# Optimization experiments

Hardware: AMD Instinct MI355X
Metric: run time of the kernel (lower is better)

Reference implementation:

```python
import jax, jax.numpy as jnp
import numpy as np

D_MODEL = 1024
NHEAD = 16
D_HEAD = D_MODEL // NHEAD


def setup_inputs() -> dict:
    key = jax.random.key(0)
    ks = jax.random.split(key, 5)
    s_in = 1.0 / np.sqrt(D_MODEL)
    x = jax.random.normal(ks[0], (2, 2048, D_MODEL), dtype=jnp.float32)
    Wqkv = jax.random.uniform(ks[1], (D_MODEL, 3 * D_MODEL), jnp.float32, -s_in, s_in)
    bqkv = jax.random.uniform(ks[2], (3 * D_MODEL,), jnp.float32, -s_in, s_in)
    Wproj = jax.random.uniform(ks[3], (D_MODEL, D_MODEL), jnp.float32, -s_in, s_in)
    bproj = jax.random.uniform(ks[4], (D_MODEL,), jnp.float32, -s_in, s_in)
    return {"x": x, "Wqkv": Wqkv, "bqkv": bqkv, "Wproj": Wproj, "bproj": bproj}


def reference(x, Wqkv, bqkv, Wproj, bproj):
    B, N, D = x.shape
    qkv = x @ Wqkv + bqkv                       # [B, N, 3D]
    q, k, v = jnp.split(qkv, 3, axis=-1)
    # [B, N, D] -> [B, H, N, d]
    def to_heads(t):
        return t.reshape(B, N, NHEAD, D_HEAD).transpose(0, 2, 1, 3)
    q, k, v = to_heads(q), to_heads(k), to_heads(v)
    scale = 1.0 / np.sqrt(D_HEAD).astype(np.float32)
    attn = jnp.einsum('bhqd,bhkd->bhqk', q, k) * scale
    attn = jax.nn.softmax(attn, axis=-1)
    y = jnp.einsum('bhqk,bhkd->bhqd', attn, v)  # [B, H, N, d]
    y = y.transpose(0, 2, 1, 3).reshape(B, N, D)
    return y @ Wproj + bproj
```

## Files before the change

### kernel.cpp

```cpp
#include <hip/hip_runtime.h>
#include <hip/hip_bf16.h>
#include <stdint.h>

typedef __hip_bfloat16 bf16;
typedef __attribute__((ext_vector_type(8))) short short8;
typedef __attribute__((ext_vector_type(4))) float f32x4;

#define QSCALE 0.18033688011f

__device__ __forceinline__ float fast_exp2(float x) {
#if __has_builtin(__builtin_amdgcn_exp2f)
  return __builtin_amdgcn_exp2f(x);
#else
  return exp2f(x);
#endif
}

__device__ __forceinline__ uint32_t pack2_bf16(float a, float b) {
#if __has_builtin(__builtin_amdgcn_cvt_pk_bf16_f32)
  typedef __attribute__((ext_vector_type(2))) __bf16 bf16x2;
  bf16x2 v = __builtin_amdgcn_cvt_pk_bf16_f32(a, b);
  return __builtin_bit_cast(uint32_t, v);
#else
  uint32_t ua = __builtin_bit_cast(uint32_t, a);
  uint32_t ub = __builtin_bit_cast(uint32_t, b);
  ua += 0x7FFF + ((ua >> 16) & 1);
  ub += 0x7FFF + ((ub >> 16) & 1);
  return (ua >> 16) | (ub & 0xFFFF0000u);
#endif
}

__device__ __forceinline__ void gload_lds16(const bf16* g, bf16* l) {
#if __has_builtin(__builtin_amdgcn_global_load_lds)
  __builtin_amdgcn_global_load_lds(
      (const __attribute__((address_space(1))) void*)(uintptr_t)g,
      (__attribute__((address_space(3))) void*)(uint32_t)(uintptr_t)l,
      16, 0, 0);
#else
  int lane = threadIdx.x & 63;
  *(short8*)(l + lane * 8) = *(const short8*)(g + lane * 8);
#endif
}

__device__ __forceinline__ void lds_barrier() {
  asm volatile("s_waitcnt lgkmcnt(0)\n\ts_barrier" ::: "memory");
}

__device__ __forceinline__ void transpose_tile(const float* __restrict__ in,
                                               bf16* __restrict__ out,
                                               int R, int C, int bx, int by,
                                               bf16 (*t)[72]) {
  const int r0 = by * 64, c0 = bx * 64;
  const int rr = threadIdx.x >> 3, cc = (threadIdx.x & 7) * 8;
#pragma unroll
  for (int rep = 0; rep < 2; ++rep) {
    int y = rr + rep * 32;
    const float* p = in + (size_t)(r0 + y) * C + c0 + cc;
    f32x4 v0 = *(const f32x4*)p;
    f32x4 v1 = *(const f32x4*)(p + 4);
#pragma unroll
    for (int j = 0; j < 4; ++j) {
      t[cc + j][y] = __float2bfloat16(v0[j]);
      t[cc + 4 + j][y] = __float2bfloat16(v1[j]);
    }
  }
  __syncthreads();
#pragma unroll
  for (int rep = 0; rep < 2; ++rep) {
    int y = rr + rep * 32;
    short8 v = *(const short8*)&t[y][cc];
    *(short8*)(out + (size_t)(c0 + y) * R + r0 + cc) = v;
  }
}

__global__ __launch_bounds__(256)
void prep_k(const float* __restrict__ x, bf16* __restrict__ xb,
            const float* __restrict__ Wqkv, bf16* __restrict__ WtQkv,
            const float* __restrict__ Wproj, bf16* __restrict__ WtP) {
  __shared__ __align__(16) bf16 t[64][72];
  const int bid = blockIdx.x;
  if (bid < 2048) {
    int i = (bid * 256 + threadIdx.x) * 8;
    f32x4 v0 = *(const f32x4*)(x + i);
    f32x4 v1 = *(const f32x4*)(x + i + 4);
    short8 r;
    bf16* rb = (bf16*)&r;
#pragma unroll
    for (int j = 0; j < 4; ++j) {
      rb[j] = __float2bfloat16(v0[j]);
      rb[4 + j] = __float2bfloat16(v1[j]);
    }
    *(short8*)(xb + i) = r;
  } else if (bid < 2048 + 768) {
    int b = bid - 2048;
    transpose_tile(Wqkv, WtQkv, 1024, 3072, b % 48, b / 48, t);
  } else {
    int b = bid - 2816;
    transpose_tile(Wproj, WtP, 1024, 1024, b % 16, b / 16, t);
  }
}

template <int MODE, int TM>
__global__ __launch_bounds__(256, 2)
void gemm_bt(const bf16* __restrict__ A, const bf16* __restrict__ Bt,
             const float* __restrict__ bias, float* __restrict__ outp,
             bf16* __restrict__ Qd, bf16* __restrict__ Kd, bf16* __restrict__ Vt,
             int M, int Nn, int K) {
  constexpr int MI = TM / 32;
  __shared__ __align__(16) bf16 As[TM * 32];
  __shared__ __align__(16) bf16 Bs[128 * 32];

  const int tid = threadIdx.x;
  const int wave = tid >> 6, lane = tid & 63;
  const int quad = lane >> 4, l16 = lane & 15;
  const int mw = (wave >> 1) * (TM / 2), nw = (wave & 1) * 64;
  const int m_blk = blockIdx.y * TM, n_blk = blockIdx.x * 128;

  f32x4 acc[MI][4];
#pragma unroll
  for (int i = 0; i < MI; ++i)
#pragma unroll
    for (int j = 0; j < 4; ++j) acc[i][j] = (f32x4){0.f, 0.f, 0.f, 0.f};

  const int rowA = lane >> 2, colA = (lane & 3) * 8;
  const int chunkB = wave * 2;
  const bf16* gB = Bt + (size_t)(n_blk + chunkB * 16 + rowA) * K + colA;
  bf16* lB0 = &Bs[chunkB * 16 * 32];
  bf16* lB1 = &Bs[(chunkB + 1) * 16 * 32];

  const int chunkA = (TM == 128) ? wave * 2 : wave;
  const bf16* gA = A + (size_t)(m_blk + chunkA * 16 + rowA) * K + colA;
  bf16* lA0 = &As[chunkA * 16 * 32];
  bf16* lA1 = &As[(chunkA + 1) * 16 * 32];

  for (int kt = 0; kt < K; kt += 32) {
    gload_lds16(gA, lA0);
    if (TM == 128) gload_lds16(gA + 16 * K, lA1);
    gload_lds16(gB, lB0);
    gload_lds16(gB + 16 * K, lB1);
    gA += 32; gB += 32;
    __syncthreads();
    short8 af[MI], bfv[4];
#pragma unroll
    for (int i = 0; i < MI; ++i)
      af[i] = *(const short8*)&As[(mw + i * 16 + l16) * 32 + quad * 8];
#pragma unroll
    for (int j = 0; j < 4; ++j)
      bfv[j] = *(const short8*)&Bs[(nw + j * 16 + l16) * 32 + quad * 8];
#pragma unroll
    for (int i = 0; i < MI; ++i)
#pragma unroll
      for (int j = 0; j < 4; ++j)
        acc[i][j] = __builtin_amdgcn_mfma_f32_16x16x32_bf16(af[i], bfv[j],
                                                            acc[i][j], 0, 0, 0);
    __syncthreads();
  }

#pragma unroll
  for (int j = 0; j < 4; ++j) {
    const int ncol = n_blk + nw + j * 16 + l16;
    const float bval = bias[ncol];
    if (MODE == 0) {
      const int part = ncol >> 10;
      const int rem = ncol & 1023;
      const int h = rem >> 6, dh = rem & 63;
#pragma unroll
      for (int i = 0; i < MI; ++i) {
        const int t0 = m_blk + mw + i * 16 + quad * 4;
        const int b = t0 >> 11, tt = t0 & 2047;
        const size_t bh = (size_t)(b * 16 + h);
        if (part == 2) {
          uint32_t w0 = pack2_bf16(acc[i][j][0] + bval, acc[i][j][1] + bval);
          uint32_t w1 = pack2_bf16(acc[i][j][2] + bval, acc[i][j][3] + bval);
          uint2 pk; pk.x = w0; pk.y = w1;
          *(uint2*)&Vt[(bh * 64 + dh) * 2048 + tt] = pk;
        } else {
          bf16* dst = (part == 0) ? Qd : Kd;
          const float sc = (part == 0) ? QSCALE : 1.0f;
#pragma unroll
          for (int r = 0; r < 4; ++r)
            dst[(bh * 2048 + tt + r) * 64 + dh] =
                __float2bfloat16((acc[i][j][r] + bval) * sc);
        }
      }
    } else {
#pragma unroll
      for (int i = 0; i < MI; ++i) {
        const int mrow0 = m_blk + mw + i * 16 + quad * 4;
#pragma unroll
        for (int r = 0; r < 4; ++r)
          outp[(size_t)(mrow0 + r) * Nn + ncol] = acc[i][j][r] + bval;
      }
    }
  }
}

__global__ __launch_bounds__(256, 3)
void attn_kernel(const bf16* __restrict__ Qg, const bf16* __restrict__ Kg,
                 const bf16* __restrict__ Vt, bf16* __restrict__ yg) {
  __shared__ __align__(16) bf16 Ks[2][64][72];
  __shared__ __align__(16) bf16 Vts[2][64 * 72];
  __shared__ __align__(16) bf16 Ps[64][72];

  const int tid = threadIdx.x;
  const int wave = tid >> 6, lane = tid & 63;
  const int quad = lane >> 4, l16 = lane & 15;
  const int qh = wave & 1, kvh = wave >> 1;

  const int bx = blockIdx.x;
  const int qt = bx & 31;
  const int bh = bx >> 5;

  const bf16* Qb = Qg + ((size_t)bh * 2048 + qt * 64) * 64;
  const bf16* Kb = Kg + (size_t)bh * 2048 * 64;
  const bf16* Vtb = Vt + (size_t)bh * 64 * 2048;

  short8 qf[2][2];
#pragma unroll
  for (int qblk = 0; qblk < 2; ++qblk)
#pragma unroll
    for (int kb = 0; kb < 2; ++kb)
      qf[qblk][kb] = *(const short8*)(
          Qb + (size_t)(qh * 32 + qblk * 16 + l16) * 64 + kb * 32 + quad * 8);

  f32x4 yacc[2][4];
#pragma unroll
  for (int qblk = 0; qblk < 2; ++qblk)
#pragma unroll
    for (int dblk = 0; dblk < 4; ++dblk)
      yacc[qblk][dblk] = (f32x4){0.f, 0.f, 0.f, 0.f};
  float sum_l[2] = {0.f, 0.f};

  const int kr = tid >> 3, kc = (tid & 7) * 8;
  const int vdd = tid & 63, vo = tid >> 6;
  const int voff0 = vdd * 72 + (((vo) + (vdd >> 3)) & 7) * 8;
  const int voff1 = vdd * 72 + (((vo + 4) + (vdd >> 3)) & 7) * 8;
  const bf16* Kp0 = Kb + (size_t)kr * 64 + kc;
  const bf16* Kp1 = Kb + (size_t)(kr + 32) * 64 + kc;
  const bf16* Vp0 = Vtb + (size_t)vdd * 2048 + vo * 8;
  const bf16* Vp1 = Vtb + (size_t)vdd * 2048 + (vo + 4) * 8;

  {
    short8 a = *(const short8*)Kp0;
    short8 b = *(const short8*)Kp1;
    short8 c = *(const short8*)Vp0;
    short8 d = *(const short8*)Vp1;
    *(short8*)&Ks[0][kr][kc] = a;
    *(short8*)&Ks[0][kr + 32][kc] = b;
    *(short8*)&Vts[0][voff0] = c;
    *(short8*)&Vts[0][voff1] = d;
  }
  short8 gk0 = *(const short8*)(Kp0 + (size_t)64 * 64);
  short8 gk1 = *(const short8*)(Kp1 + (size_t)64 * 64);
  short8 gv0 = *(const short8*)(Vp0 + 64);
  short8 gv1 = *(const short8*)(Vp1 + 64);
  __syncthreads();

  for (int kt = 0; kt < 2048; kt += 64) {
    const int cur = (kt >> 6) & 1;

    if (kt + 64 < 2048) {
      *(short8*)&Ks[cur ^ 1][kr][kc] = gk0;
      *(short8*)&Ks[cur ^ 1][kr + 32][kc] = gk1;
      *(short8*)&Vts[cur ^ 1][voff0] = gv0;
      *(short8*)&Vts[cur ^ 1][voff1] = gv1;
      if (kt + 128 < 2048) {
        gk0 = *(const short8*)(Kp0 + (size_t)(kt + 128) * 64);
        gk1 = *(const short8*)(Kp1 + (size_t)(kt + 128) * 64);
        gv0 = *(const short8*)(Vp0 + kt + 128);
        gv1 = *(const short8*)(Vp1 + kt + 128);
      }
    }

    f32x4 st[2][2];
#pragma unroll
    for (int kvblk = 0; kvblk < 2; ++kvblk) {
      const int krow = kvh * 32 + kvblk * 16 + l16;
      short8 kf0 = *(const short8*)&Ks[cur][krow][quad * 8];
      short8 kf1 = *(const short8*)&Ks[cur][krow][32 + quad * 8];
#pragma unroll
      for (int qblk = 0; qblk < 2; ++qblk) {
        f32x4 a = (f32x4){0.f, 0.f, 0.f, 0.f};
        a = __builtin_amdgcn_mfma_f32_16x16x32_bf16(kf0, qf[qblk][0], a, 0, 0, 0);
        a = __builtin_amdgcn_mfma_f32_16x16x32_bf16(kf1, qf[qblk][1], a, 0, 0, 0);
        st[qblk][kvblk] = a;
      }
    }

#pragma unroll
    for (int qblk = 0; qblk < 2; ++qblk) {
      float ssum = 0.f;
#pragma unroll
      for (int kvblk = 0; kvblk < 2; ++kvblk) {
        float p0 = fast_exp2(st[qblk][kvblk][0]);
        float p1 = fast_exp2(st[qblk][kvblk][1]);
        float p2 = fast_exp2(st[qblk][kvblk][2]);
        float p3 = fast_exp2(st[qblk][kvblk][3]);
        ssum += (p0 + p1) + (p2 + p3);
        uint2 pk;
        pk.x = pack2_bf16(p0, p1);
        pk.y = pack2_bf16(p2, p3);
        *(uint2*)&Ps[qh * 32 + qblk * 16 + l16]
                    [kvh * 32 + kvblk * 16 + quad * 4] = pk;
      }
      sum_l[qblk] += ssum;
    }

    lds_barrier();

    short8 vbf[4];
#pragma unroll
    for (int dblk = 0; dblk < 4; ++dblk) {
      const int d = dblk * 16 + l16;
      vbf[dblk] = *(const short8*)&Vts[cur][d * 72 +
          (((kvh * 4 + quad) + (d >> 3)) & 7) * 8];
    }
#pragma unroll
    for (int qblk = 0; qblk < 2; ++qblk) {
      short8 pa = *(const short8*)&Ps[qh * 32 + qblk * 16 + l16]
                                     [kvh * 32 + quad * 8];
#pragma unroll
      for (int dblk = 0; dblk < 4; ++dblk)
        yacc[qblk][dblk] = __builtin_amdgcn_mfma_f32_16x16x32_bf16(
            pa, vbf[dblk], yacc[qblk][dblk], 0, 0, 0);
    }

    lds_barrier();
  }

#pragma unroll
  for (int qblk = 0; qblk < 2; ++qblk) {
    sum_l[qblk] += __shfl_xor(sum_l[qblk], 16);
    sum_l[qblk] += __shfl_xor(sum_l[qblk], 32);
  }
  __syncthreads();
  float* red = (float*)&Ks[0][0][0];
  float* sred = (float*)&Ps[0][0];
  if (kvh == 1) {
#pragma unroll
    for (int qblk = 0; qblk < 2; ++qblk) {
#pragma unroll
      for (int dblk = 0; dblk < 4; ++dblk) {
        const int f = (qh * 2 + qblk) * 4 + dblk;
        *(f32x4*)&red[(f * 64 + quad * 16 + l16) * 4] = yacc[qblk][dblk];
      }
      if (quad == 0) sred[(qh * 2 + qblk) * 16 + l16] = sum_l[qblk];
    }
  }
  __syncthreads();
  if (kvh == 0) {
    const int b = bh >> 4, h = bh & 15;
    const size_t rowbase = (size_t)b * 2048 + qt * 64;
#pragma unroll
    for (int qblk = 0; qblk < 2; ++qblk) {
      sum_l[qblk] += sred[(qh * 2 + qblk) * 16 + l16];
#pragma unroll
      for (int dblk = 0; dblk < 4; ++dblk) {
        const int f = (qh * 2 + qblk) * 4 + dblk;
        f32x4 o = *(const f32x4*)&red[(f * 64 + quad * 16 + l16) * 4];
#pragma unroll
        for (int r = 0; r < 4; ++r) yacc[qblk][dblk][r] += o[r];
      }
#pragma unroll
      for (int r = 0; r < 4; ++r) {
        const float lv = __shfl(sum_l[qblk], quad * 4 + r, 16);
        const float inv = 1.f / lv;
        const int rr = qh * 32 + qblk * 16 + quad * 4 + r;
#pragma unroll
        for (int dblk = 0; dblk < 4; ++dblk)
          yg[(rowbase + rr) * 1024 + h * 64 + dblk * 16 + l16] =
              __float2bfloat16(yacc[qblk][dblk][r] * inv);
      }
    }
  }
}

extern "C" void kernel_launch(void* const* d_in, const int* in_sizes, int n_in,
                              void* d_out, int out_size, void* d_ws, size_t ws_size,
                              hipStream_t stream) {
  const float* x = (const float*)d_in[0];
  const float* Wqkv = (const float*)d_in[1];
  const float* bqkv = (const float*)d_in[2];
  const float* Wproj = (const float*)d_in[3];
  const float* bproj = (const float*)d_in[4];
  float* out = (float*)d_out;

  if (ws_size < (size_t)40 * 1024 * 1024) return;

  char* ws = (char*)d_ws;
  bf16* xb    = (bf16*)(ws + 0);
  bf16* yd    = (bf16*)(ws + 0);
  bf16* WtQkv = (bf16*)(ws + 8388608);
  bf16* WtP   = (bf16*)(ws + 14680064);
  bf16* Qd    = (bf16*)(ws + 16777216);
  bf16* Kd    = (bf16*)(ws + 25165824);
  bf16* Vten  = (bf16*)(ws + 33554432);

  prep_k<<<3072, 256, 0, stream>>>(x, xb, Wqkv, WtQkv, Wproj, WtP);
  gemm_bt<0, 128><<<dim3(24, 32), 256, 0, stream>>>(
      xb, WtQkv, bqkv, nullptr, Qd, Kd, Vten, 4096, 3072, 1024);
  attn_kernel<<<dim3(1024), 256, 0, stream>>>(Qd, Kd, Vten, yd);
  gemm_bt<1, 64><<<dim3(8, 64), 256, 0, stream>>>(
      yd, WtP, bproj, out, nullptr, nullptr, nullptr, 4096, 1024, 1024);
}
```

Before: 200.6 us.

## Stage QKV GEMM epilogue through LDS for coalesced stores; single-buffer K in attention

The QKV GEMM epilogue now writes each head's tile into shared memory, then stores Q/K rows and transposed V rows to global memory with 16-byte coalesced writes, replacing scattered 2-byte and 8-byte stores. The attention kernel drops K double-buffering: K is written into a single LDS buffer after the QK barrier. This frees LDS so the occupancy hint can rise from 3 to 4 blocks. The cost is extra barriers and LDS traffic in the epilogue, and a shorter window to hide K load latency.

```diff
diff --git a/kernel.cpp b/kernel.cpp
--- a/kernel.cpp
+++ b/kernel.cpp
@@ -107,8 +107,9 @@
              bf16* __restrict__ Qd, bf16* __restrict__ Kd, bf16* __restrict__ Vt,
              int M, int Nn, int K) {
   constexpr int MI = TM / 32;
-  __shared__ __align__(16) bf16 As[TM * 32];
-  __shared__ __align__(16) bf16 Bs[128 * 32];
+  __shared__ __align__(16) bf16 smem[(TM == 128) ? 9216 : 6144];
+  bf16* As = smem;
+  bf16* Bs = smem + TM * 32;
 
   const int tid = threadIdx.x;
   const int wave = tid >> 6, lane = tid & 63;
@@ -156,34 +157,73 @@
     __syncthreads();
   }
 
-#pragma unroll
-  for (int j = 0; j < 4; ++j) {
-    const int ncol = n_blk + nw + j * 16 + l16;
-    const float bval = bias[ncol];
-    if (MODE == 0) {
-      const int part = ncol >> 10;
-      const int rem = ncol & 1023;
-      const int h = rem >> 6, dh = rem & 63;
-#pragma unroll
-      for (int i = 0; i < MI; ++i) {
-        const int t0 = m_blk + mw + i * 16 + quad * 4;
-        const int b = t0 >> 11, tt = t0 & 2047;
-        const size_t bh = (size_t)(b * 16 + h);
+  if (MODE == 0) {
+    float bval[4];
+#pragma unroll
+    for (int j = 0; j < 4; ++j) bval[j] = bias[n_blk + nw + j * 16 + l16];
+
+    const int part = n_blk >> 10;
+    const int b = m_blk >> 11;
+    const int tloc = m_blk & 2047;
+    const int h0 = (n_blk & 1023) >> 6;
+
+#pragma unroll
+    for (int p = 0; p < 2; ++p) {
+      __syncthreads();
+      if ((nw >> 6) == p) {
         if (part == 2) {
-          uint32_t w0 = pack2_bf16(acc[i][j][0] + bval, acc[i][j][1] + bval);
-          uint32_t w1 = pack2_bf16(acc[i][j][2] + bval, acc[i][j][3] + bval);
-          uint2 pk; pk.x = w0; pk.y = w1;
-          *(uint2*)&Vt[(bh * 64 + dh) * 2048 + tt] = pk;
+#pragma unroll
+          for (int i = 0; i < MI; ++i)
+#pragma unroll
+            for (int j = 0; j < 4; ++j) {
+              const int dh = j * 16 + l16;
+              const int t0 = mw + i * 16 + quad * 4;
+              uint2 pk;
+              pk.x = pack2_bf16(acc[i][j][0] + bval[j], acc[i][j][1] + bval[j]);
+              pk.y = pack2_bf16(acc[i][j][2] + bval[j], acc[i][j][3] + bval[j]);
+              *(uint2*)&smem[dh * 136 + t0] = pk;
+            }
         } else {
-          bf16* dst = (part == 0) ? Qd : Kd;
           const float sc = (part == 0) ? QSCALE : 1.0f;
 #pragma unroll
-          for (int r = 0; r < 4; ++r)
-            dst[(bh * 2048 + tt + r) * 64 + dh] =
-                __float2bfloat16((acc[i][j][r] + bval) * sc);
+          for (int i = 0; i < MI; ++i)
+#pragma unroll
+            for (int j = 0; j < 4; ++j) {
+              const int d = j * 16 + l16;
+              const int t0 = mw + i * 16 + quad * 4;
+#pragma unroll
+              for (int r = 0; r < 4; ++r)
+                smem[(t0 + r) * 72 + d] =
+                    __float2bfloat16((acc[i][j][r] + bval[j]) * sc);
+            }
         }
       }
-    } else {
+      __syncthreads();
+      const size_t bh = (size_t)(b * 16 + h0 + p);
+      if (part == 2) {
+#pragma unroll
+        for (int it = 0; it < 4; ++it) {
+          const int dl = (tid >> 4) + it * 16;
+          const int t8 = (tid & 15) * 8;
+          short8 v = *(const short8*)&smem[dl * 136 + t8];
+          *(short8*)&Vt[(bh * 64 + dl) * 2048 + tloc + t8] = v;
+        }
+      } else {
+        bf16* dst = (part == 0) ? Qd : Kd;
+#pragma unroll
+        for (int it = 0; it < 4; ++it) {
+          const int row = (tid >> 3) + it * 32;
+          const int col8 = (tid & 7) * 8;
+          short8 v = *(const short8*)&smem[row * 72 + col8];
+          *(short8*)&dst[(bh * 2048 + tloc + row) * 64 + col8] = v;
+        }
+      }
+    }
+  } else {
+#pragma unroll
+    for (int j = 0; j < 4; ++j) {
+      const int ncol = n_blk + nw + j * 16 + l16;
+      const float bval = bias[ncol];
 #pragma unroll
       for (int i = 0; i < MI; ++i) {
         const int mrow0 = m_blk + mw + i * 16 + quad * 4;
@@ -195,10 +235,10 @@
   }
 }
 
-__global__ __launch_bounds__(256, 3)
+__global__ __launch_bounds__(256, 4)
 void attn_kernel(const bf16* __restrict__ Qg, const bf16* __restrict__ Kg,
                  const bf16* __restrict__ Vt, bf16* __restrict__ yg) {
-  __shared__ __align__(16) bf16 Ks[2][64][72];
+  __shared__ __align__(16) bf16 Ks[64][72];
   __shared__ __align__(16) bf16 Vts[2][64 * 72];
   __shared__ __align__(16) bf16 Ps[64][72];
 
@@ -245,8 +285,8 @@
     short8 b = *(const short8*)Kp1;
     short8 c = *(const short8*)Vp0;
     short8 d = *(const short8*)Vp1;
-    *(short8*)&Ks[0][kr][kc] = a;
-    *(short8*)&Ks[0][kr + 32][kc] = b;
+    *(short8*)&Ks[kr][kc] = a;
+    *(short8*)&Ks[kr + 32][kc] = b;
     *(short8*)&Vts[0][voff0] = c;
     *(short8*)&Vts[0][voff1] = d;
   }
@@ -260,13 +300,9 @@
     const int cur = (kt >> 6) & 1;
 
     if (kt + 64 < 2048) {
-      *(short8*)&Ks[cur ^ 1][kr][kc] = gk0;
-      *(short8*)&Ks[cur ^ 1][kr + 32][kc] = gk1;
       *(short8*)&Vts[cur ^ 1][voff0] = gv0;
       *(short8*)&Vts[cur ^ 1][voff1] = gv1;
       if (kt + 128 < 2048) {
-        gk0 = *(const short8*)(Kp0 + (size_t)(kt + 128) * 64);
-        gk1 = *(const short8*)(Kp1 + (size_t)(kt + 128) * 64);
         gv0 = *(const short8*)(Vp0 + kt + 128);
         gv1 = *(const short8*)(Vp1 + kt + 128);
       }
@@ -276,8 +312,8 @@
 #pragma unroll
     for (int kvblk = 0; kvblk < 2; ++kvblk) {
       const int krow = kvh * 32 + kvblk * 16 + l16;
-      short8 kf0 = *(const short8*)&Ks[cur][krow][quad * 8];
-      short8 kf1 = *(const short8*)&Ks[cur][krow][32 + quad * 8];
+      short8 kf0 = *(const short8*)&Ks[krow][quad * 8];
+      short8 kf1 = *(const short8*)&Ks[krow][32 + quad * 8];
 #pragma unroll
       for (int qblk = 0; qblk < 2; ++qblk) {
         f32x4 a = (f32x4){0.f, 0.f, 0.f, 0.f};
@@ -308,6 +344,15 @@
 
     lds_barrier();
 
+    if (kt + 64 < 2048) {
+      *(short8*)&Ks[kr][kc] = gk0;
+      *(short8*)&Ks[kr + 32][kc] = gk1;
+      if (kt + 128 < 2048) {
+        gk0 = *(const short8*)(Kp0 + (size_t)(kt + 128) * 64);
+        gk1 = *(const short8*)(Kp1 + (size_t)(kt + 128) * 64);
+      }
+    }
+
     short8 vbf[4];
 #pragma unroll
     for (int dblk = 0; dblk < 4; ++dblk) {
@@ -334,7 +379,7 @@
     sum_l[qblk] += __shfl_xor(sum_l[qblk], 32);
   }
   __syncthreads();
-  float* red = (float*)&Ks[0][0][0];
+  float* red = (float*)&Vts[0][0];
   float* sred = (float*)&Ps[0][0];
   if (kvh == 1) {
 #pragma unroll
```

Result: faster. 195.8 us (-2.4%).
